# Kernel tuning notes

Hardware: AMD Instinct MI355X
Metric: run time of the kernel (lower is better)

## Reference

```python
import jax, jax.numpy as jnp
import numpy as np

EMBED = 2048
HQ = 32
HKV = 8
HD = EMBED // HQ          # 64
G = HQ // HKV             # 4 q heads per kv head
SCALE = 1.0 / np.sqrt(EMBED)  # module uses 1/sqrt(embed_dim), not head_dim
B, S = 4, 2048


def setup_inputs() -> dict:
    key = jax.random.key(0)
    ks = jax.random.split(key, 10)
    x = jax.random.normal(ks[0], (B, S, EMBED), dtype=jnp.float32)
    # RoPE tables: theta=10000, angles[t, i] = t / theta^(2i/HD)
    inv_freq = 1.0 / (10000.0 ** (jnp.arange(0, HD, 2, dtype=jnp.float32) / HD))  # [HD/2]
    angles = jnp.arange(S, dtype=jnp.float32)[:, None] * inv_freq[None, :]        # [S, HD/2]
    freqs_cos = jnp.cos(angles)
    freqs_sin = jnp.sin(angles)
    s = 0.02
    wq_w = jax.random.normal(ks[1], (EMBED, EMBED), jnp.float32) * s
    wq_b = jnp.zeros((EMBED,), jnp.float32)
    wk_w = jax.random.normal(ks[2], (HKV * HD, EMBED), jnp.float32) * s
    wk_b = jnp.zeros((HKV * HD,), jnp.float32)
    wv_w = jax.random.normal(ks[3], (HKV * HD, EMBED), jnp.float32) * s
    wv_b = jnp.zeros((HKV * HD,), jnp.float32)
    wo_w = jax.random.normal(ks[4], (EMBED, EMBED), jnp.float32) * s
    wo_b = jnp.zeros((EMBED,), jnp.float32)
    return dict(x=x, freqs_cos=freqs_cos, freqs_sin=freqs_sin,
                wq_w=wq_w, wq_b=wq_b, wk_w=wk_w, wk_b=wk_b,
                wv_w=wv_w, wv_b=wv_b, wo_w=wo_w, wo_b=wo_b)


def _rope(t, cos, sin):
    # t: [B, S, H, HD]; cos/sin: [S, HD/2] -> broadcast [1, S, 1, HD/2]
    tr = t[..., 0::2]
    ti = t[..., 1::2]
    c = cos[None, :, None, :]
    s = sin[None, :, None, :]
    out_r = tr * c - ti * s
    out_i = tr * s + ti * c
    # interleave back to [..., HD]
    return jnp.stack([out_r, out_i], axis=-1).reshape(t.shape)


def _forward(x, freqs_cos, freqs_sin, wq_w, wq_b, wk_w, wk_b, wv_w, wv_b, wo_w, wo_b):
    b, s, _ = x.shape
    q = (x @ wq_w.T + wq_b).reshape(b, s, HQ, HD)
    k = (x @ wk_w.T + wk_b).reshape(b, s, HKV, HD)
    v = (x @ wv_w.T + wv_b).reshape(b, s, HKV, HD)
    q = _rope(q, freqs_cos, freqs_sin)
    k = _rope(k, freqs_cos, freqs_sin)
    # GQA: group q heads as [HKV, G] instead of repeat_interleave'ing k/v
    qg = q.reshape(b, s, HKV, G, HD)
    scores = jnp.einsum('bqhgd,bkhd->bhgqk', qg, k) * SCALE  # [B,HKV,G,S,S]
    causal = jnp.tril(jnp.ones((s, s), dtype=bool))
    scores = jnp.where(causal, scores, jnp.finfo(scores.dtype).min)
    p = jax.nn.softmax(scores, axis=-1)
    o = jnp.einsum('bhgqk,bkhd->bqhgd', p, v).reshape(b, s, EMBED)
    return o @ wo_w.T + wo_b


def reference(x, freqs_cos, freqs_sin, wq_w, wq_b, wk_w, wk_b, wv_w, wv_b, wo_w, wo_b):
    return _forward(x, freqs_cos, freqs_sin, wq_w, wq_b, wk_w, wk_b,
                    wv_w, wv_b, wo_w, wo_b)
```

## Files before the change

### kernel.cpp

```cpp
#include <hip/hip_runtime.h>
#include <stdint.h>

typedef unsigned short u16;
typedef __attribute__((ext_vector_type(8))) short bf16x8;
typedef __attribute__((ext_vector_type(4))) float f32x4;

#define MFMA_BF16(a,b,c) __builtin_amdgcn_mfma_f32_16x16x32_bf16((a),(b),(c),0,0,0)

#define GLOAD_LDS16(g, l) \
  __builtin_amdgcn_global_load_lds((const __attribute__((address_space(1))) void*)(g), \
                                   (__attribute__((address_space(3))) void*)(l), 16, 0, 0)

__device__ inline u16 f2bf(float f) {
  uint32_t u = __builtin_bit_cast(uint32_t, f);
  u = (u + 0x7FFFu + ((u >> 16) & 1u)) >> 16;
  return (u16)u;
}
__device__ inline float bf2f(u16 h) {
  uint32_t u = ((uint32_t)h) << 16;
  return __builtin_bit_cast(float, u);
}

__global__ __launch_bounds__(256) void cvt_kernel(const float* __restrict__ src,
                                                  u16* __restrict__ dst, int n4) {
  int i = blockIdx.x * 256 + threadIdx.x;
  if (i >= n4) return;
  float4 v = reinterpret_cast<const float4*>(src)[i];
  uint2 o;
  o.x = (uint32_t)f2bf(v.x) | ((uint32_t)f2bf(v.y) << 16);
  o.y = (uint32_t)f2bf(v.z) | ((uint32_t)f2bf(v.w) << 16);
  reinterpret_cast<uint2*>(dst)[i] = o;
}

template<typename OutT>
__global__ __launch_bounds__(256) void gemm_bt(
    const u16* __restrict__ A, const u16* __restrict__ B,
    const float* __restrict__ bias, OutT* __restrict__ C,
    int M, int N, int K)
{
  __shared__ u16 As[128 * 64];
  __shared__ u16 Bs[128 * 64];
  const int bm = blockIdx.y, bn = blockIdx.x;
  const int tid = threadIdx.x;
  const int lane = tid & 63;
  const int wv = tid >> 6;
  const int wm = wv >> 1, wn = wv & 1;
  const int g = lane >> 4, qn = lane & 15;

  f32x4 acc[4][4];
  #pragma unroll
  for (int i = 0; i < 4; ++i)
    #pragma unroll
    for (int j = 0; j < 4; ++j) acc[i][j] = (f32x4){0.f, 0.f, 0.f, 0.f};

  const u16* Ab = A + (size_t)bm * 128 * K;
  const u16* Bb = B + (size_t)bn * 128 * K;
  const int lr = lane >> 3, lc = lane & 7;

  for (int kt = 0; kt < K; kt += 64) {
    __syncthreads();
    #pragma unroll
    for (int i = 0; i < 4; ++i) {
      int r0 = wv * 32 + i * 8;
      size_t goff = (size_t)(r0 + lr) * K + kt + lc * 8;
      GLOAD_LDS16(Ab + goff, As + r0 * 64);
      GLOAD_LDS16(Bb + goff, Bs + r0 * 64);
    }
    __syncthreads();
    #pragma unroll
    for (int ks = 0; ks < 2; ++ks) {
      bf16x8 af[4], bfr[4];
      #pragma unroll
      for (int mi = 0; mi < 4; ++mi)
        af[mi] = *reinterpret_cast<const bf16x8*>(As + (wm * 64 + mi * 16 + qn) * 64 + g * 8 + ks * 32);
      #pragma unroll
      for (int ni = 0; ni < 4; ++ni)
        bfr[ni] = *reinterpret_cast<const bf16x8*>(Bs + (wn * 64 + ni * 16 + qn) * 64 + g * 8 + ks * 32);
      #pragma unroll
      for (int mi = 0; mi < 4; ++mi)
        #pragma unroll
        for (int ni = 0; ni < 4; ++ni)
          acc[mi][ni] = MFMA_BF16(af[mi], bfr[ni], acc[mi][ni]);
    }
  }
  #pragma unroll
  for (int ni = 0; ni < 4; ++ni) {
    int col = bn * 128 + wn * 64 + ni * 16 + qn;
    float bs = bias[col];
    #pragma unroll
    for (int mi = 0; mi < 4; ++mi) {
      #pragma unroll
      for (int r = 0; r < 4; ++r) {
        int row = bm * 128 + wm * 64 + mi * 16 + g * 4 + r;
        float v = acc[mi][ni][r] + bs;
        if constexpr (sizeof(OutT) == 2) C[(size_t)row * N + col] = (OutT)f2bf(v);
        else                             C[(size_t)row * N + col] = v;
      }
    }
  }
}

__global__ __launch_bounds__(256) void rope_kernel(
    u16* __restrict__ T, const float* __restrict__ cosT, const float* __restrict__ sinT,
    int heads8, int n8)
{
  int i = blockIdx.x * 256 + threadIdx.x;
  if (i >= n8) return;
  int tok = i / heads8;
  int r = i - tok * heads8;
  int d0 = (r & 7) * 8;
  int s = tok & 2047;
  uint4 v = reinterpret_cast<uint4*>(T)[i];
  u16* e = reinterpret_cast<u16*>(&v);
  float4 c = *reinterpret_cast<const float4*>(cosT + s * 32 + d0 / 2);
  float4 sn = *reinterpret_cast<const float4*>(sinT + s * 32 + d0 / 2);
  float cc[4] = {c.x, c.y, c.z, c.w}, ss[4] = {sn.x, sn.y, sn.z, sn.w};
  #pragma unroll
  for (int j = 0; j < 4; ++j) {
    float tr = bf2f(e[2 * j]), ti = bf2f(e[2 * j + 1]);
    e[2 * j]     = f2bf(tr * cc[j] - ti * ss[j]);
    e[2 * j + 1] = f2bf(tr * ss[j] + ti * cc[j]);
  }
  reinterpret_cast<uint4*>(T)[i] = v;
}

__global__ __launch_bounds__(256) void attn_kernel(
    const u16* __restrict__ Q, const u16* __restrict__ Kb,
    const u16* __restrict__ Vb, u16* __restrict__ O)
{
  constexpr float SCALE = 0.02209708691207961f;
  __shared__ u16 Kl[2][64 * 64];
  __shared__ u16 Vt[2][64 * 64];
  __shared__ u16 Pl[4][16 * 64];
  const int qt = blockIdx.x, hq = blockIdx.y, b = blockIdx.z;
  const int kvh = hq >> 2;
  const int tid = threadIdx.x, lane = tid & 63, w = tid >> 6;
  const int g = lane >> 4, qn = lane & 15;
  const int sw = qn & 7;
  const int q_g = qt * 64 + w * 16 + qn;

  const u16* qrow = Q + ((size_t)(b * 2048 + q_g) * 2048 + hq * 64);
  bf16x8 qf[2];
  qf[0] = *reinterpret_cast<const bf16x8*>(qrow + g * 8);
  qf[1] = *reinterpret_cast<const bf16x8*>(qrow + g * 8 + 32);
  #pragma unroll
  for (int i = 0; i < 2; ++i)
    #pragma unroll
    for (int j = 0; j < 8; ++j)
      qf[i][j] = (short)f2bf(bf2f((u16)qf[i][j]) * SCALE);

  bool dmask[4];
  #pragma unroll
  for (int r = 0; r < 4; ++r) dmask[r] = (g * 4 + r) > qn;

  float m = -1e30f, l = 0.f;
  f32x4 oa[4];
  #pragma unroll
  for (int i = 0; i < 4; ++i) oa[i] = (f32x4){0.f, 0.f, 0.f, 0.f};

  const u16* Kbase = Kb + ((size_t)b * 2048 * 512 + kvh * 64);
  const u16* Vbase = Vb + ((size_t)b * 2048 * 512 + kvh * 64);
  const int nkt = qt + 1;
  const int lr = lane >> 3, lc = lane & 7;
  const int csw = lc ^ (lr & 7);

  #pragma unroll
  for (int i = 0; i < 2; ++i) {
    int r0 = w * 16 + i * 8;
    GLOAD_LDS16(Kbase + (size_t)(r0 + lr) * 512 + csw * 8, &Kl[0][r0 * 64]);
  }
  #pragma unroll
  for (int i = 0; i < 2; ++i) {
    int rc = w + 4 * i;
    uint4 pk; u16* t = (u16*)&pk;
    #pragma unroll
    for (int j = 0; j < 8; ++j)
      t[j] = Vbase[(size_t)(rc * 8 + j) * 512 + lane];
    int slot = rc ^ (lane & 7);
    *reinterpret_cast<uint4*>(&Vt[0][lane * 64 + slot * 8]) = pk;
  }
  __syncthreads();

  int cur = 0;
  for (int kt = 0; kt < nkt; ++kt) {
    const bool haveNext = (kt + 1 < nkt);
    const bool last = (kt == nkt - 1);
    uint4 vr[2];
    if (haveNext) {
      #pragma unroll
      for (int i = 0; i < 2; ++i) {
        int r0 = w * 16 + i * 8;
        GLOAD_LDS16(Kbase + (size_t)((kt + 1) * 64 + r0 + lr) * 512 + csw * 8,
                    &Kl[cur ^ 1][r0 * 64]);
      }
      #pragma unroll
      for (int i = 0; i < 2; ++i) {
        int rc = w + 4 * i;
        u16* t = (u16*)&vr[i];
        #pragma unroll
        for (int j = 0; j < 8; ++j)
          t[j] = Vbase[(size_t)((kt + 1) * 64 + rc * 8 + j) * 512 + lane];
      }
    }

    const u16* Kc = Kl[cur];
    f32x4 st[4];
    #pragma unroll
    for (int cf = 0; cf < 4; ++cf) st[cf] = (f32x4){0.f, 0.f, 0.f, 0.f};
    #pragma unroll
    for (int cf = 0; cf < 4; ++cf) {
      if (last && cf > w) continue;
      #pragma unroll
      for (int ks = 0; ks < 2; ++ks) {
        int slot = (g + 4 * ks) ^ sw;
        bf16x8 kf = *reinterpret_cast<const bf16x8*>(Kc + (cf * 16 + qn) * 64 + slot * 8);
        st[cf] = MFMA_BF16(kf, qf[ks], st[cf]);
      }
    }

    float pv[16];
    float tmax = -1e30f;
    #pragma unroll
    for (int cf = 0; cf < 4; ++cf) {
      if (last && cf > w) {
        #pragma unroll
        for (int r = 0; r < 4; ++r) pv[cf * 4 + r] = 0.f;
      } else if (last && cf == w) {
        #pragma unroll
        for (int r = 0; r < 4; ++r) {
          float s = dmask[r] ? -1e30f : st[cf][r];
          pv[cf * 4 + r] = s; tmax = fmaxf(tmax, s);
        }
      } else {
        #pragma unroll
        for (int r = 0; r < 4; ++r) {
          float s = st[cf][r];
          pv[cf * 4 + r] = s; tmax = fmaxf(tmax, s);
        }
      }
    }
    tmax = fmaxf(tmax, __shfl_xor(tmax, 16));
    tmax = fmaxf(tmax, __shfl_xor(tmax, 32));
    float mnew = fmaxf(m, tmax);
    float fac = __expf(m - mnew);
    float lsum = 0.f;
    #pragma unroll
    for (int cf = 0; cf < 4; ++cf) {
      if (last && cf > w) continue;
      #pragma unroll
      for (int r = 0; r < 4; ++r) {
        float p = __expf(pv[cf * 4 + r] - mnew);
        pv[cf * 4 + r] = p; lsum += p;
      }
    }
    lsum += __shfl_xor(lsum, 16);
    lsum += __shfl_xor(lsum, 32);
    l = l * fac + lsum;
    m = mnew;
    #pragma unroll
    for (int r = 0; r < 4; ++r) {
      float fr = __shfl(fac, (lane & 48) | (g * 4 + r));
      #pragma unroll
      for (int df = 0; df < 4; ++df) oa[df][r] *= fr;
    }

    u16* Pw = Pl[w];
    #pragma unroll
    for (int cf = 0; cf < 4; ++cf) {
      uint32_t lo = (uint32_t)f2bf(pv[cf * 4 + 0]) | ((uint32_t)f2bf(pv[cf * 4 + 1]) << 16);
      uint32_t hi = (uint32_t)f2bf(pv[cf * 4 + 2]) | ((uint32_t)f2bf(pv[cf * 4 + 3]) << 16);
      int slot = (2 * cf + (g >> 1)) ^ sw;
      uint2 u2; u2.x = lo; u2.y = hi;
      *reinterpret_cast<uint2*>(Pw + qn * 64 + slot * 8 + (g & 1) * 4) = u2;
    }

    if (haveNext) {
      #pragma unroll
      for (int i = 0; i < 2; ++i) {
        int rc = w + 4 * i;
        int slot = rc ^ (lane & 7);
        *reinterpret_cast<uint4*>(&Vt[cur ^ 1][lane * 64 + slot * 8]) = vr[i];
      }
    }

    const u16* Vc = Vt[cur];
    #pragma unroll
    for (int ks = 0; ks < 2; ++ks) {
      int slotp = (g + 4 * ks) ^ sw;
      bf16x8 pa = *reinterpret_cast<const bf16x8*>(Pw + qn * 64 + slotp * 8);
      #pragma unroll
      for (int df = 0; df < 4; ++df) {
        bf16x8 vf = *reinterpret_cast<const bf16x8*>(Vc + (df * 16 + qn) * 64 + slotp * 8);
        oa[df] = MFMA_BF16(pa, vf, oa[df]);
      }
    }
    __syncthreads();
    cur ^= 1;
  }

  #pragma unroll
  for (int r = 0; r < 4; ++r) {
    float lrv = __shfl(l, (lane & 48) | (g * 4 + r));
    float inv = 1.f / lrv;
    int row_g = qt * 64 + w * 16 + g * 4 + r;
    u16* orow = O + ((size_t)(b * 2048 + row_g) * 2048 + hq * 64);
    #pragma unroll
    for (int df = 0; df < 4; ++df)
      orow[df * 16 + qn] = f2bf(oa[df][r] * inv);
  }
}

extern "C" void kernel_launch(void* const* d_in, const int* in_sizes, int n_in,
                              void* d_out, int out_size, void* d_ws, size_t ws_size,
                              hipStream_t stream) {
  const float* x    = (const float*)d_in[0];
  const float* fc   = (const float*)d_in[1];
  const float* fs   = (const float*)d_in[2];
  const float* wq_w = (const float*)d_in[3];
  const float* wq_b = (const float*)d_in[4];
  const float* wk_w = (const float*)d_in[5];
  const float* wk_b = (const float*)d_in[6];
  const float* wv_w = (const float*)d_in[7];
  const float* wv_b = (const float*)d_in[8];
  const float* wo_w = (const float*)d_in[9];
  const float* wo_b = (const float*)d_in[10];
  float* out = (float*)d_out;
  char* ws = (char*)d_ws;

  const size_t NEEDED = 96468992;
  if (ws_size < NEEDED) return;

  u16* x_bf  = (u16*)(ws);
  u16* Qb    = (u16*)(ws + 33554432);
  u16* Kb    = (u16*)(ws + 67108864);
  u16* Vb    = (u16*)(ws + 75497472);
  u16* Wbuf  = (u16*)(ws + 83886080);
  u16* wk_bf = (u16*)(ws + 92274688);
  u16* wv_bf = (u16*)(ws + 94371840);
  u16* Ob    = x_bf;

  cvt_kernel<<<16384, 256, 0, stream>>>(x,    x_bf, 4194304);
  cvt_kernel<<< 4096, 256, 0, stream>>>(wq_w, Wbuf, 1048576);
  cvt_kernel<<< 1024, 256, 0, stream>>>(wk_w, wk_bf, 262144);
  cvt_kernel<<< 1024, 256, 0, stream>>>(wv_w, wv_bf, 262144);

  gemm_bt<u16><<<dim3(16, 64), 256, 0, stream>>>(x_bf, Wbuf,  wq_b, Qb, 8192, 2048, 2048);
  gemm_bt<u16><<<dim3( 4, 64), 256, 0, stream>>>(x_bf, wk_bf, wk_b, Kb, 8192,  512, 2048);
  gemm_bt<u16><<<dim3( 4, 64), 256, 0, stream>>>(x_bf, wv_bf, wv_b, Vb, 8192,  512, 2048);

  cvt_kernel<<< 4096, 256, 0, stream>>>(wo_w, Wbuf, 1048576);

  rope_kernel<<<8192, 256, 0, stream>>>(Qb, fc, fs, 256, 2097152);
  rope_kernel<<<2048, 256, 0, stream>>>(Kb, fc, fs,  64,  524288);

  attn_kernel<<<dim3(32, 32, 4), 256, 0, stream>>>(Qb, Kb, Vb, Ob);

  gemm_bt<float><<<dim3(16, 64), 256, 0, stream>>>(Ob, Wbuf, wo_b, out, 8192, 2048, 2048);
}
```

Measured before the change: 782.8 us.

## Enlarge attention query tile to 128 rows and fuse Q RoPE into attention

Each attention block now handles 128 query rows, two 16-row sub-tiles per wave, so every loaded K/V tile is reused by twice as many queries and the grid is halved. Query RoPE and the softmax scale (folded with log2e) are applied when Q is loaded, which removes the separate Q rope pass. Softmax uses a raw v_exp_f32 (exp2) and bf16 conversion uses the library intrinsic. Per-diagonal masking skips fully masked MFMAs. The cost is higher register pressure (launch bounds set to 3) and larger shared memory for P.

```diff
diff --git a/kernel.cpp b/kernel.cpp
--- a/kernel.cpp
+++ b/kernel.cpp
@@ -1,4 +1,5 @@
 #include <hip/hip_runtime.h>
+#include <hip/hip_bf16.h>
 #include <stdint.h>
 
 typedef unsigned short u16;
@@ -12,13 +13,14 @@
                                    (__attribute__((address_space(3))) void*)(l), 16, 0, 0)
 
 __device__ inline u16 f2bf(float f) {
-  uint32_t u = __builtin_bit_cast(uint32_t, f);
-  u = (u + 0x7FFFu + ((u >> 16) & 1u)) >> 16;
-  return (u16)u;
+  return __builtin_bit_cast(u16, __float2bfloat16(f));
 }
 __device__ inline float bf2f(u16 h) {
   uint32_t u = ((uint32_t)h) << 16;
   return __builtin_bit_cast(float, u);
+}
+__device__ inline float exp2a(float x) {
+  float r; asm("v_exp_f32 %0, %1" : "=v"(r) : "v"(x)); return r;
 }
 
 __global__ __launch_bounds__(256) void cvt_kernel(const float* __restrict__ src,
@@ -124,174 +126,210 @@
   reinterpret_cast<uint4*>(T)[i] = v;
 }
 
-__global__ __launch_bounds__(256) void attn_kernel(
+__global__ __launch_bounds__(256, 3) void attn_kernel(
     const u16* __restrict__ Q, const u16* __restrict__ Kb,
-    const u16* __restrict__ Vb, u16* __restrict__ O)
+    const u16* __restrict__ Vb, const float* __restrict__ cosT,
+    const float* __restrict__ sinT, u16* __restrict__ O)
 {
-  constexpr float SCALE = 0.02209708691207961f;
+  constexpr float SCALE2 = 0.02209708691207961f * 1.4426950408889634f;
   __shared__ u16 Kl[2][64 * 64];
   __shared__ u16 Vt[2][64 * 64];
-  __shared__ u16 Pl[4][16 * 64];
+  __shared__ u16 Pl[4][32 * 64];
   const int qt = blockIdx.x, hq = blockIdx.y, b = blockIdx.z;
   const int kvh = hq >> 2;
   const int tid = threadIdx.x, lane = tid & 63, w = tid >> 6;
   const int g = lane >> 4, qn = lane & 15;
   const int sw = qn & 7;
-  const int q_g = qt * 64 + w * 16 + qn;
-
-  const u16* qrow = Q + ((size_t)(b * 2048 + q_g) * 2048 + hq * 64);
-  bf16x8 qf[2];
-  qf[0] = *reinterpret_cast<const bf16x8*>(qrow + g * 8);
-  qf[1] = *reinterpret_cast<const bf16x8*>(qrow + g * 8 + 32);
-  #pragma unroll
-  for (int i = 0; i < 2; ++i)
-    #pragma unroll
-    for (int j = 0; j < 8; ++j)
-      qf[i][j] = (short)f2bf(bf2f((u16)qf[i][j]) * SCALE);
-
-  bool dmask[4];
-  #pragma unroll
-  for (int r = 0; r < 4; ++r) dmask[r] = (g * 4 + r) > qn;
-
-  float m = -1e30f, l = 0.f;
-  f32x4 oa[4];
-  #pragma unroll
-  for (int i = 0; i < 4; ++i) oa[i] = (f32x4){0.f, 0.f, 0.f, 0.f};
+
+  bf16x8 qf[2][2];
+  #pragma unroll
+  for (int a = 0; a < 2; ++a) {
+    int qg = qt * 128 + w * 32 + a * 16 + qn;
+    const u16* qrow = Q + ((size_t)(b * 2048 + qg) * 2048 + hq * 64);
+    #pragma unroll
+    for (int ks = 0; ks < 2; ++ks) {
+      bf16x8 raw = *reinterpret_cast<const bf16x8*>(qrow + ks * 32 + g * 8);
+      float4 c4 = *reinterpret_cast<const float4*>(cosT + qg * 32 + ks * 16 + g * 4);
+      float4 s4 = *reinterpret_cast<const float4*>(sinT + qg * 32 + ks * 16 + g * 4);
+      float cc[4] = {c4.x, c4.y, c4.z, c4.w}, ssv[4] = {s4.x, s4.y, s4.z, s4.w};
+      bf16x8 o;
+      #pragma unroll
+      for (int t = 0; t < 4; ++t) {
+        float tr = bf2f((u16)raw[2 * t]), ti = bf2f((u16)raw[2 * t + 1]);
+        o[2 * t]     = (short)f2bf((tr * cc[t] - ti * ssv[t]) * SCALE2);
+        o[2 * t + 1] = (short)f2bf((tr * ssv[t] + ti * cc[t]) * SCALE2);
+      }
+      qf[a][ks] = o;
+    }
+  }
+
+  float m[2] = {-3.0e38f, -3.0e38f}, l[2] = {0.f, 0.f};
+  f32x4 oa[2][4];
+  #pragma unroll
+  for (int a = 0; a < 2; ++a)
+    #pragma unroll
+    for (int df = 0; df < 4; ++df) oa[a][df] = (f32x4){0.f, 0.f, 0.f, 0.f};
 
   const u16* Kbase = Kb + ((size_t)b * 2048 * 512 + kvh * 64);
   const u16* Vbase = Vb + ((size_t)b * 2048 * 512 + kvh * 64);
-  const int nkt = qt + 1;
   const int lr = lane >> 3, lc = lane & 7;
   const int csw = lc ^ (lr & 7);
 
+  const u16* kp0 = Kbase + (size_t)(w * 16 + lr) * 512 + csw * 8;
+  const u16* kp1 = kp0 + 8 * 512;
+  const u16* vpA[2]; const u16* vpB[2];
   #pragma unroll
   for (int i = 0; i < 2; ++i) {
-    int r0 = w * 16 + i * 8;
-    GLOAD_LDS16(Kbase + (size_t)(r0 + lr) * 512 + csw * 8, &Kl[0][r0 * 64]);
-  }
+    int rc = w + 4 * i;
+    vpA[i] = Vbase + (size_t)(rc * 8) * 512 + lane;
+    vpB[i] = vpA[i] + 4 * 512;
+  }
+
+  GLOAD_LDS16(kp0, &Kl[0][(w * 16) * 64]);
+  GLOAD_LDS16(kp1, &Kl[0][(w * 16 + 8) * 64]);
+  kp0 += 32768; kp1 += 32768;
   #pragma unroll
   for (int i = 0; i < 2; ++i) {
     int rc = w + 4 * i;
     uint4 pk; u16* t = (u16*)&pk;
     #pragma unroll
-    for (int j = 0; j < 8; ++j)
-      t[j] = Vbase[(size_t)(rc * 8 + j) * 512 + lane];
+    for (int j = 0; j < 4; ++j) { t[j] = vpA[i][j * 512]; t[4 + j] = vpB[i][j * 512]; }
+    vpA[i] += 32768; vpB[i] += 32768;
     int slot = rc ^ (lane & 7);
     *reinterpret_cast<uint4*>(&Vt[0][lane * 64 + slot * 8]) = pk;
   }
   __syncthreads();
 
+  const int nkt = 2 * qt + 2;
   int cur = 0;
   for (int kt = 0; kt < nkt; ++kt) {
     const bool haveNext = (kt + 1 < nkt);
-    const bool last = (kt == nkt - 1);
-    uint4 vr[2];
+    uint4 vr0, vr1;
     if (haveNext) {
-      #pragma unroll
-      for (int i = 0; i < 2; ++i) {
-        int r0 = w * 16 + i * 8;
-        GLOAD_LDS16(Kbase + (size_t)((kt + 1) * 64 + r0 + lr) * 512 + csw * 8,
-                    &Kl[cur ^ 1][r0 * 64]);
-      }
-      #pragma unroll
-      for (int i = 0; i < 2; ++i) {
-        int rc = w + 4 * i;
-        u16* t = (u16*)&vr[i];
-        #pragma unroll
-        for (int j = 0; j < 8; ++j)
-          t[j] = Vbase[(size_t)((kt + 1) * 64 + rc * 8 + j) * 512 + lane];
-      }
+      GLOAD_LDS16(kp0, &Kl[cur ^ 1][(w * 16) * 64]);
+      GLOAD_LDS16(kp1, &Kl[cur ^ 1][(w * 16 + 8) * 64]);
+      kp0 += 32768; kp1 += 32768;
+      u16* t0 = (u16*)&vr0; u16* t1 = (u16*)&vr1;
+      #pragma unroll
+      for (int j = 0; j < 4; ++j) { t0[j] = vpA[0][j * 512]; t0[4 + j] = vpB[0][j * 512]; }
+      vpA[0] += 32768; vpB[0] += 32768;
+      #pragma unroll
+      for (int j = 0; j < 4; ++j) { t1[j] = vpA[1][j * 512]; t1[4 + j] = vpB[1][j * 512]; }
+      vpA[1] += 32768; vpB[1] += 32768;
     }
 
     const u16* Kc = Kl[cur];
-    f32x4 st[4];
-    #pragma unroll
-    for (int cf = 0; cf < 4; ++cf) st[cf] = (f32x4){0.f, 0.f, 0.f, 0.f};
+    const int ddb = kt * 64 - (qt * 128 + w * 32);
+    f32x4 st[2][4];
+    #pragma unroll
+    for (int a = 0; a < 2; ++a)
+      #pragma unroll
+      for (int cf = 0; cf < 4; ++cf) st[a][cf] = (f32x4){0.f, 0.f, 0.f, 0.f};
+
     #pragma unroll
     for (int cf = 0; cf < 4; ++cf) {
-      if (last && cf > w) continue;
-      #pragma unroll
-      for (int ks = 0; ks < 2; ++ks) {
-        int slot = (g + 4 * ks) ^ sw;
-        bf16x8 kf = *reinterpret_cast<const bf16x8*>(Kc + (cf * 16 + qn) * 64 + slot * 8);
-        st[cf] = MFMA_BF16(kf, qf[ks], st[cf]);
-      }
-    }
-
-    float pv[16];
-    float tmax = -1e30f;
-    #pragma unroll
-    for (int cf = 0; cf < 4; ++cf) {
-      if (last && cf > w) {
-        #pragma unroll
-        for (int r = 0; r < 4; ++r) pv[cf * 4 + r] = 0.f;
-      } else if (last && cf == w) {
+      int dd0 = ddb + cf * 16;
+      int dd1 = dd0 - 16;
+      if (dd1 >= 16) continue;
+      bf16x8 kf0 = *reinterpret_cast<const bf16x8*>(Kc + (cf * 16 + qn) * 64 + ((g) ^ sw) * 8);
+      bf16x8 kf1 = *reinterpret_cast<const bf16x8*>(Kc + (cf * 16 + qn) * 64 + ((g + 4) ^ sw) * 8);
+      if (dd0 < 16) {
+        st[0][cf] = MFMA_BF16(kf0, qf[0][0], st[0][cf]);
+        st[0][cf] = MFMA_BF16(kf1, qf[0][1], st[0][cf]);
+      }
+      st[1][cf] = MFMA_BF16(kf0, qf[1][0], st[1][cf]);
+      st[1][cf] = MFMA_BF16(kf1, qf[1][1], st[1][cf]);
+    }
+
+    float fac[2]; bool doP[2];
+    #pragma unroll
+    for (int a = 0; a < 2; ++a) {
+      int dda = ddb - a * 16;
+      doP[a] = (dda < 16);
+      fac[a] = 1.f;
+      if (!doP[a]) continue;
+      float tmax = -3.0e38f;
+      #pragma unroll
+      for (int cf = 0; cf < 4; ++cf) {
+        int dd = dda + cf * 16;
+        if (dd >= 16) continue;
+        if (dd > -16) {
+          int thr = qn - dd;
+          #pragma unroll
+          for (int r = 0; r < 4; ++r) {
+            float s = (g * 4 + r > thr) ? -3.0e38f : st[a][cf][r];
+            st[a][cf][r] = s;
+            tmax = fmaxf(tmax, s);
+          }
+        } else {
+          #pragma unroll
+          for (int r = 0; r < 4; ++r) tmax = fmaxf(tmax, st[a][cf][r]);
+        }
+      }
+      tmax = fmaxf(tmax, __shfl_xor(tmax, 16));
+      tmax = fmaxf(tmax, __shfl_xor(tmax, 32));
+      float mnew = fmaxf(m[a], tmax);
+      fac[a] = exp2a(m[a] - mnew);
+      float lsum = 0.f;
+      #pragma unroll
+      for (int cf = 0; cf < 4; ++cf) {
+        int dd = dda + cf * 16;
+        if (dd >= 16) continue;
         #pragma unroll
         for (int r = 0; r < 4; ++r) {
-          float s = dmask[r] ? -1e30f : st[cf][r];
-          pv[cf * 4 + r] = s; tmax = fmaxf(tmax, s);
+          float p = exp2a(st[a][cf][r] - mnew);
+          st[a][cf][r] = p;
+          lsum += p;
         }
-      } else {
+      }
+      lsum += __shfl_xor(lsum, 16);
+      lsum += __shfl_xor(lsum, 32);
+      l[a] = l[a] * fac[a] + lsum;
+      m[a] = mnew;
+      #pragma unroll
+      for (int r = 0; r < 4; ++r) {
+        float fr = __shfl(fac[a], (lane & 48) | (g * 4 + r));
         #pragma unroll
-        for (int r = 0; r < 4; ++r) {
-          float s = st[cf][r];
-          pv[cf * 4 + r] = s; tmax = fmaxf(tmax, s);
-        }
-      }
-    }
-    tmax = fmaxf(tmax, __shfl_xor(tmax, 16));
-    tmax = fmaxf(tmax, __shfl_xor(tmax, 32));
-    float mnew = fmaxf(m, tmax);
-    float fac = __expf(m - mnew);
-    float lsum = 0.f;
-    #pragma unroll
-    for (int cf = 0; cf < 4; ++cf) {
-      if (last && cf > w) continue;
-      #pragma unroll
-      for (int r = 0; r < 4; ++r) {
-        float p = __expf(pv[cf * 4 + r] - mnew);
-        pv[cf * 4 + r] = p; lsum += p;
-      }
-    }
-    lsum += __shfl_xor(lsum, 16);
-    lsum += __shfl_xor(lsum, 32);
-    l = l * fac + lsum;
-    m = mnew;
-    #pragma unroll
-    for (int r = 0; r < 4; ++r) {
-      float fr = __shfl(fac, (lane & 48) | (g * 4 + r));
-      #pragma unroll
-      for (int df = 0; df < 4; ++df) oa[df][r] *= fr;
+        for (int df = 0; df < 4; ++df) oa[a][df][r] *= fr;
+      }
     }
 
     u16* Pw = Pl[w];
     #pragma unroll
-    for (int cf = 0; cf < 4; ++cf) {
-      uint32_t lo = (uint32_t)f2bf(pv[cf * 4 + 0]) | ((uint32_t)f2bf(pv[cf * 4 + 1]) << 16);
-      uint32_t hi = (uint32_t)f2bf(pv[cf * 4 + 2]) | ((uint32_t)f2bf(pv[cf * 4 + 3]) << 16);
-      int slot = (2 * cf + (g >> 1)) ^ sw;
-      uint2 u2; u2.x = lo; u2.y = hi;
-      *reinterpret_cast<uint2*>(Pw + qn * 64 + slot * 8 + (g & 1) * 4) = u2;
+    for (int a = 0; a < 2; ++a) {
+      if (!doP[a]) continue;
+      #pragma unroll
+      for (int cf = 0; cf < 4; ++cf) {
+        uint32_t lo = (uint32_t)f2bf(st[a][cf][0]) | ((uint32_t)f2bf(st[a][cf][1]) << 16);
+        uint32_t hi = (uint32_t)f2bf(st[a][cf][2]) | ((uint32_t)f2bf(st[a][cf][3]) << 16);
+        int slot = (2 * cf + (g >> 1)) ^ sw;
+        uint2 u2; u2.x = lo; u2.y = hi;
+        *reinterpret_cast<uint2*>(Pw + (a * 16 + qn) * 64 + slot * 8 + (g & 1) * 4) = u2;
+      }
     }
 
     if (haveNext) {
-      #pragma unroll
-      for (int i = 0; i < 2; ++i) {
-        int rc = w + 4 * i;
-        int slot = rc ^ (lane & 7);
-        *reinterpret_cast<uint4*>(&Vt[cur ^ 1][lane * 64 + slot * 8]) = vr[i];
-      }
+      int slot0 = w ^ (lane & 7);
+      int slot1 = (w + 4) ^ (lane & 7);
+      *reinterpret_cast<uint4*>(&Vt[cur ^ 1][lane * 64 + slot0 * 8]) = vr0;
+      *reinterpret_cast<uint4*>(&Vt[cur ^ 1][lane * 64 + slot1 * 8]) = vr1;
     }
 
     const u16* Vc = Vt[cur];
     #pragma unroll
     for (int ks = 0; ks < 2; ++ks) {
-      int slotp = (g + 4 * ks) ^ sw;
-      bf16x8 pa = *reinterpret_cast<const bf16x8*>(Pw + qn * 64 + slotp * 8);
-      #pragma unroll
-      for (int df = 0; df < 4; ++df) {
-        bf16x8 vf = *reinterpret_cast<const bf16x8*>(Vc + (df * 16 + qn) * 64 + slotp * 8);
-        oa[df] = MFMA_BF16(pa, vf, oa[df]);
+      int slotv = (g + 4 * ks) ^ sw;
+      bf16x8 vf[4];
+      #pragma unroll
+      for (int df = 0; df < 4; ++df)
+        vf[df] = *reinterpret_cast<const bf16x8*>(Vc + (df * 16 + qn) * 64 + slotv * 8);
+      #pragma unroll
+      for (int a = 0; a < 2; ++a) {
+        if (!doP[a]) continue;
+        bf16x8 pa = *reinterpret_cast<const bf16x8*>(Pw + (a * 16 + qn) * 64 + slotv * 8);
+        #pragma unroll
+        for (int df = 0; df < 4; ++df)
+          oa[a][df] = MFMA_BF16(pa, vf[df], oa[a][df]);
       }
     }
     __syncthreads();
@@ -299,14 +337,17 @@
   }
 
   #pragma unroll
-  for (int r = 0; r < 4; ++r) {
-    float lrv = __shfl(l, (lane & 48) | (g * 4 + r));
-    float inv = 1.f / lrv;
-    int row_g = qt * 64 + w * 16 + g * 4 + r;
-    u16* orow = O + ((size_t)(b * 2048 + row_g) * 2048 + hq * 64);
-    #pragma unroll
-    for (int df = 0; df < 4; ++df)
-      orow[df * 16 + qn] = f2bf(oa[df][r] * inv);
+  for (int a = 0; a < 2; ++a) {
+    #pragma unroll
+    for (int r = 0; r < 4; ++r) {
+      float lrv = __shfl(l[a], (lane & 48) | (g * 4 + r));
+      float inv = 1.f / lrv;
+      int row_g = qt * 128 + w * 32 + a * 16 + g * 4 + r;
+      u16* orow = O + ((size_t)(b * 2048 + row_g) * 2048 + hq * 64);
+      #pragma unroll
+      for (int df = 0; df < 4; ++df)
+        orow[df * 16 + qn] = f2bf(oa[a][df][r] * inv);
+    }
   }
 }
 
@@ -350,10 +391,9 @@
 
   cvt_kernel<<< 4096, 256, 0, stream>>>(wo_w, Wbuf, 1048576);
 
-  rope_kernel<<<8192, 256, 0, stream>>>(Qb, fc, fs, 256, 2097152);
-  rope_kernel<<<2048, 256, 0, stream>>>(Kb, fc, fs,  64,  524288);
-
-  attn_kernel<<<dim3(32, 32, 4), 256, 0, stream>>>(Qb, Kb, Vb, Ob);
+  rope_kernel<<<2048, 256, 0, stream>>>(Kb, fc, fs, 64, 524288);
+
+  attn_kernel<<<dim3(16, 32, 4), 256, 0, stream>>>(Qb, Kb, Vb, fc, fs, Ob);
 
   gemm_bt<float><<<dim3(16, 64), 256, 0, stream>>>(Ob, Wbuf, wo_b, out, 8192, 2048, 2048);
 }
```

Result: faster. 728.6 us (-6.9%).
